# Optimization experiments

Hardware: AMD Instinct MI355X
Metric: run time of the kernel (lower is better)

Reference implementation:

```python
import jax, jax.numpy as jnp
import numpy as np

B, T, D_IN = 64, 256, 256
H, N, W, R, D_OUT = 512, 128, 64, 4, 256
CTRL_IN = D_IN + R * W          # 512
IFACE = R * W + R + W + 1 + W + W + R * 3  # 465
EPS = 1e-8


def setup_inputs() -> dict:
    key = jax.random.key(0)
    ks = jax.random.split(key, 10)
    def lin(k, out_d, in_d):
        s = 1.0 / np.sqrt(in_d)
        return jax.random.uniform(k, (out_d, in_d), jnp.float32, -s, s)
    def vec(k, d, in_d):
        s = 1.0 / np.sqrt(in_d)
        return jax.random.uniform(k, (d,), jnp.float32, -s, s)
    return {
        'x': jax.random.normal(ks[0], (B, T, D_IN), jnp.float32),
        'W_ih': lin(ks[1], 4 * H, CTRL_IN),
        'W_hh': lin(ks[2], 4 * H, H),
        'b_ih': vec(ks[3], 4 * H, H),
        'b_hh': vec(ks[4], 4 * H, H),
        'W_int': lin(ks[5], IFACE, H),
        'b_int': vec(ks[6], IFACE, H),
        'W_out': lin(ks[7], D_OUT, H + R * W),
        'b_out': vec(ks[8], D_OUT, H + R * W),
    }


def _content_weights(mem, keys, strength):
    # mem: (b, n, w); keys: (b, r, w); strength: (b, r, 1) -> weights (b, r, n)
    dot = jnp.einsum('brw,bnw->brn', keys, mem)
    nm = jnp.maximum(jnp.linalg.norm(mem, axis=-1), EPS)      # (b, n)
    nk = jnp.maximum(jnp.linalg.norm(keys, axis=-1), EPS)     # (b, r)
    sim = dot / (nk[:, :, None] * nm[:, None, :])
    return jax.nn.softmax(strength * sim, axis=-1)


def reference(x, W_ih, W_hh, b_ih, b_hh, W_int, b_int, W_out, b_out):
    b = x.shape[0]

    def step(carry, x_t):
        h, c, mem, rv = carry
        ci = jnp.concatenate([x_t, rv.reshape(b, R * W)], axis=-1)
        gates = ci @ W_ih.T + b_ih + h @ W_hh.T + b_hh
        i_g, f_g, g_g, o_g = jnp.split(gates, 4, axis=-1)  # torch LSTM gate order
        c = jax.nn.sigmoid(f_g) * c + jax.nn.sigmoid(i_g) * jnp.tanh(g_g)
        h = jax.nn.sigmoid(o_g) * jnp.tanh(c)

        iface = h @ W_int.T + b_int
        idx = 0
        read_keys = iface[:, idx:idx + R * W].reshape(b, R, W); idx += R * W
        read_str = jax.nn.softplus(iface[:, idx:idx + R]) + 1.0; idx += R
        write_key = iface[:, idx:idx + W]; idx += W
        write_str = jax.nn.softplus(iface[:, idx:idx + 1]) + 1.0; idx += 1
        erase = jax.nn.sigmoid(iface[:, idx:idx + W]); idx += W
        write_vec = iface[:, idx:idx + W]; idx += W
        # read_modes are parsed in the original but never used -> skipped

        ww = _content_weights(mem, write_key[:, None, :], write_str[:, None, :])[:, 0, :]  # (b, n)
        mem = mem * (1.0 - ww[:, :, None] * erase[:, None, :]) + ww[:, :, None] * write_vec[:, None, :]

        rw = _content_weights(mem, read_keys, read_str[:, :, None])  # (b, r, n)
        rv = jnp.einsum('brn,bnw->brw', rw, mem)

        out = jnp.concatenate([h, rv.reshape(b, R * W)], axis=-1) @ W_out.T + b_out
        return (h, c, mem, rv), out

    init = (jnp.zeros((b, H), x.dtype), jnp.zeros((b, H), x.dtype),
            jnp.zeros((b, N, W), x.dtype), jnp.zeros((b, R, W), x.dtype))
    _, outs = jax.lax.scan(step, init, jnp.swapaxes(x, 0, 1))  # outs: (T, b, D_OUT)
    return outs[-1]  # return_sequence=False -> last timestep
```

## Files before the change

### kernel.cpp

```cpp
#include <hip/hip_runtime.h>
#include <math.h>

#define BB_   64
#define TT_   256
#define DIN_  256
#define HH_   512
#define NMEM_ 128
#define WWID_ 64
#define RR_   4
#define DOUT_ 256
#define CTRL_ 512
#define EPSV  1e-8f
#define NBLK  256
#define NTHR  512
#define OSTR  456
#define MPAD  65

__device__ __forceinline__ float sigm(float x){ return 1.f/(1.f+expf(-x)); }
__device__ __forceinline__ float softp(float x){ return (x>20.f)? x : log1pf(expf(x)); }
__device__ __forceinline__ float wredsum(float v){
  #pragma unroll
  for (int o=32;o>0;o>>=1) v += __shfl_xor(v,o,64);
  return v;
}
__device__ __forceinline__ float wredmax(float v){
  #pragma unroll
  for (int o=32;o>0;o>>=1) v = fmaxf(v, __shfl_xor(v,o,64));
  return v;
}

__device__ __forceinline__ float2 cload2(const float* p){
  unsigned long long u = __hip_atomic_load((const unsigned long long*)p,
                          __ATOMIC_RELAXED, __HIP_MEMORY_SCOPE_AGENT);
  float2 r; __builtin_memcpy(&r, &u, 8); return r;
}
__device__ __forceinline__ void cstore2(float* p, float2 v){
  unsigned long long u; __builtin_memcpy(&u, &v, 8);
  __hip_atomic_store((unsigned long long*)p, u, __ATOMIC_RELAXED,
                     __HIP_MEMORY_SCOPE_AGENT);
}
__device__ __forceinline__ void cstore1(float* p, float v){
  unsigned u; __builtin_memcpy(&u, &v, 4);
  __hip_atomic_store((unsigned*)p, u, __ATOMIC_RELAXED, __HIP_MEMORY_SCOPE_AGENT);
}

__device__ __forceinline__ void gridbar(unsigned* bar, unsigned k)
{
  __syncthreads();
  if (threadIdx.x == 0) {
    const int g = blockIdx.x >> 3;
    unsigned a = __hip_atomic_fetch_add(bar + g*32, 1u, __ATOMIC_RELAXED,
                                        __HIP_MEMORY_SCOPE_AGENT);
    bool released = false;
    if (a == 8u*k - 1u) {
      unsigned r = __hip_atomic_fetch_add(bar + 1024, 1u, __ATOMIC_RELAXED,
                                          __HIP_MEMORY_SCOPE_AGENT);
      if (r == 32u*k - 1u) {
        __hip_atomic_store(bar + 1056, k, __ATOMIC_RELAXED,
                           __HIP_MEMORY_SCOPE_AGENT);
        released = true;
      }
    }
    if (!released) {
      while (__hip_atomic_load(bar + 1056, __ATOMIC_RELAXED,
                               __HIP_MEMORY_SCOPE_AGENT) < k)
        __builtin_amdgcn_s_sleep(1);
    }
  }
  __syncthreads();
}

__global__ void k_initbar(unsigned* bar){
  int i = blockIdx.x*256 + threadIdx.x;
  if (i < 1088)
    __hip_atomic_store(bar + i, 0u, __ATOMIC_RELAXED, __HIP_MEMORY_SCOPE_AGENT);
}

__global__ void k_prep_w(const float* __restrict__ Wint, float* __restrict__ WiT4){
  const int o  = blockIdx.x;
  const int kq = threadIdx.x;
  float4 v = *(const float4*)(Wint + (size_t)o*HH_ + 4*kq);
  *(float4*)(WiT4 + ((size_t)kq*OSTR + o)*4) = v;
}

struct Params {
  const float *x, *Wih, *Whh, *bih, *bhh, *bint, *Wout, *bout;
  float *out;
  float *hp;
  float *rvp;
  float *WiT4;
  unsigned *bar;
};

union __align__(16) SMu {
  struct {
    float4 actS[2048];
    float  red[4][4][16][8];
  } a;
  float redO[4][4][64];
  struct {
    float hS[HH_];
    float ifcS[OSTR];
    float kpk[WWID_][8];
    float dH[4][NMEM_];
    float qH[4][NMEM_];
    float nH[4][NMEM_];
    float drH[4][RR_][NMEM_];
    float wwS[NMEM_];
    float rwS[RR_][NMEM_];
    float rvH[8][64];
    float scal[8];
    float red2[8];
  } c;
};

__launch_bounds__(NTHR, 2)
__global__ void k_persist(Params p)
{
  __shared__ SMu sm;
  __shared__ float memS[NMEM_][MPAD];

  const int bi  = blockIdx.x;
  const int tid = threadIdx.x;
  const int b   = tid & 63;
  const int wv  = tid >> 6;
  const int rg  = bi & 31;
  const int col = bi >> 5;
  const int j0  = rg*16;
  const int B0  = col*8;
  const int bb  = bi;

  const int ksA = tid >> 7;
  const int jlA = (tid >> 3) & 15;
  const int blA = tid & 7;

  float c_reg = 0.f;

  const float* wbg[4];
  {
    const float* wsrc = (ksA < 2) ? p.Wih : p.Whh;
    const int koff = (ksA & 1) * 256;
    #pragma unroll
    for (int g = 0; g < 4; ++g)
      wbg[g] = wsrc + (size_t)(g*HH_ + j0 + jlA)*CTRL_ + koff;
  }

  float bsum[4];
  if (tid < 128) {
    const int j = j0 + (tid >> 3);
    #pragma unroll
    for (int g = 0; g < 4; ++g)
      bsum[g] = p.bih[g*HH_ + j] + p.bhh[g*HH_ + j];
  }
  float bintR = 0.f;
  if (bi < 64 && tid < 453) bintR = p.bint[tid];

  {
    const float2 zz = make_float2(0.f, 0.f);
    const int gt = bi*NTHR + tid;
    if      (gt < 16384) cstore2(p.hp  + 2*gt,         zz);
    else if (gt < 24576) cstore2(p.rvp + 2*(gt-16384), zz);
    if (bi < 64)
      for (int i = tid; i < NMEM_*MPAD; i += NTHR)
        ((float*)memS)[i] = 0.f;
  }
  unsigned bk = 1;
  gridbar(p.bar, bk);

  for (int t = 0; t < TT_; ++t) {
    const int cur = t & 1, nxt = cur ^ 1;
    const float* hR = p.hp + cur*32768;
    float*       hW = p.hp + nxt*32768;

    {
      #pragma unroll
      for (int i = 0; i < 4; ++i) {
        const int idx = tid + 512*i;
        const int kq = idx >> 3, bl = idx & 7, bg = B0 + bl;
        float4 v;
        if (kq < 64) {
          v = *(const float4*)(p.x + (size_t)bg*(TT_*DIN_)
                               + (size_t)t*DIN_ + kq*4);
        } else if (kq < 128) {
          const float* s = p.rvp + (kq-64)*256 + bg*4;
          float2 lo = cload2(s), hi = cload2(s + 2);
          v = make_float4(lo.x, lo.y, hi.x, hi.y);
        } else {
          const float* s = hR + (kq-128)*256 + bg*4;
          float2 lo = cload2(s), hi = cload2(s + 2);
          v = make_float4(lo.x, lo.y, hi.x, hi.y);
        }
        sm.a.actS[idx] = v;
      }
      __syncthreads();

      float4 ac[4];
      #pragma unroll
      for (int g = 0; g < 4; ++g) ac[g] = make_float4(0.f, 0.f, 0.f, 0.f);

      const int kbase = ksA*64;
      #pragma unroll 4
      for (int i = 0; i < 64; ++i) {
        float4 a = sm.a.actS[(kbase + i)*8 + blA];
        #pragma unroll
        for (int g = 0; g < 4; ++g) {
          float4 w = *(const float4*)(wbg[g] + (i << 2));
          ac[g].x += w.x*a.x; ac[g].y += w.y*a.y;
          ac[g].z += w.z*a.z; ac[g].w += w.w*a.w;
        }
      }
      #pragma unroll
      for (int g = 0; g < 4; ++g)
        sm.a.red[ksA][g][jlA][blA] = (ac[g].x + ac[g].y) + (ac[g].z + ac[g].w);
      __syncthreads();

      if (tid < 128) {
        const int jl = tid >> 3, bl = tid & 7;
        float gs[4];
        #pragma unroll
        for (int g = 0; g < 4; ++g)
          gs[g] = sm.a.red[0][g][jl][bl] + sm.a.red[1][g][jl][bl]
                + sm.a.red[2][g][jl][bl] + sm.a.red[3][g][jl][bl] + bsum[g];
        float cn = sigm(gs[1])*c_reg + sigm(gs[0])*tanhf(gs[2]);
        c_reg = cn;
        float hn = sigm(gs[3])*tanhf(cn);
        const int j = j0 + jl, bg = B0 + bl;
        cstore1(hW + (j>>2)*256 + bg*4 + (j&3), hn);
      }
    }
    gridbar(p.bar, ++bk);

    if (bi < 64) {
      if (tid < 128) {
        const float* hsrc = hW + tid*256 + bb*4;
        float2 lo = cload2(hsrc), hi = cload2(hsrc + 2);
        sm.c.hS[4*tid]   = lo.x; sm.c.hS[4*tid+1] = lo.y;
        sm.c.hS[4*tid+2] = hi.x; sm.c.hS[4*tid+3] = hi.y;
      }
      __syncthreads();
      {
        const int o = (tid < 453) ? tid : 452;
        float a0 = bintR, a1 = 0.f, a2 = 0.f, a3 = 0.f;
        #pragma unroll 8
        for (int kq = 0; kq < 128; ++kq) {
          float4 w  = *(const float4*)(p.WiT4 + ((size_t)kq*OSTR + o)*4);
          float4 h4 = *(const float4*)&sm.c.hS[kq << 2];
          a0 += w.x*h4.x; a1 += w.y*h4.y; a2 += w.z*h4.z; a3 += w.w*h4.w;
        }
        if (tid < 453) sm.c.ifcS[tid] = (a0 + a1) + (a2 + a3);
      }
      __syncthreads();

      if (tid < 64) {
        const int w = tid;
        float wk = sm.c.ifcS[260+w];
        float q0 = sm.c.ifcS[w],      q1 = sm.c.ifcS[64+w];
        float q2 = sm.c.ifcS[128+w],  q3 = sm.c.ifcS[192+w];
        float er  = sigm(sm.c.ifcS[325+w]);
        float wvc = sm.c.ifcS[389+w];
        sm.c.kpk[w][0]=wk; sm.c.kpk[w][1]=q0; sm.c.kpk[w][2]=q1; sm.c.kpk[w][3]=q2;
        sm.c.kpk[w][4]=q3; sm.c.kpk[w][5]=er; sm.c.kpk[w][6]=wvc; sm.c.kpk[w][7]=0.f;
        float s0 = wredsum(wk*wk);
        float s1 = wredsum(q0*q0);
        float s2 = wredsum(q1*q1);
        float s3 = wredsum(q2*q2);
        float s4 = wredsum(q3*q3);
        if (w == 0) {
          sm.c.scal[0] = fmaxf(sqrtf(s0), EPSV);
          sm.c.scal[1] = fmaxf(sqrtf(s1), EPSV);
          sm.c.scal[2] = fmaxf(sqrtf(s2), EPSV);
          sm.c.scal[3] = fmaxf(sqrtf(s3), EPSV);
          sm.c.scal[4] = fmaxf(sqrtf(s4), EPSV);
        }
      }
      __syncthreads();

      const int n  = tid & 127;
      const int wh = tid >> 7;

      {
        float dotw = 0.f, q = 0.f;
        const int w0 = wh*16;
        #pragma unroll
        for (int w = 0; w < 16; ++w) {
          float m = memS[n][w0+w];
          dotw += sm.c.kpk[w0+w][0]*m;
          q    += m*m;
        }
        sm.c.dH[wh][n] = dotw;
        sm.c.qH[wh][n] = q;
      }
      __syncthreads();

      float a_n = 0.f, e_n = 0.f;
      const float wstr = softp(sm.c.ifcS[324]) + 1.f;
      if (tid < 128) {
        float dot = sm.c.dH[0][n] + sm.c.dH[1][n] + sm.c.dH[2][n] + sm.c.dH[3][n];
        float q2  = sm.c.qH[0][n] + sm.c.qH[1][n] + sm.c.qH[2][n] + sm.c.qH[3][n];
        a_n = wstr * dot / (sm.c.scal[0] * fmaxf(sqrtf(q2), EPSV));
        float mx = wredmax(a_n);
        if ((tid & 63) == 0) sm.c.red2[tid>>6] = mx;
      }
      __syncthreads();
      if (tid < 128) {
        float mx = fmaxf(sm.c.red2[0], sm.c.red2[1]);
        e_n = expf(a_n - mx);
        float s = wredsum(e_n);
        if ((tid & 63) == 0) sm.c.red2[4 + (tid>>6)] = s;
      }
      __syncthreads();
      if (tid < 128)
        sm.c.wwS[n] = e_n / (sm.c.red2[4] + sm.c.red2[5]);
      __syncthreads();

      {
        float ww_n = sm.c.wwS[n];
        float nrm=0.f, d0=0.f, d1=0.f, d2=0.f, d3=0.f;
        const int w0 = wh*16;
        #pragma unroll
        for (int w = 0; w < 16; ++w) {
          float4 k0 = *(const float4*)&sm.c.kpk[w0+w][0];
          float4 k1 = *(const float4*)&sm.c.kpk[w0+w][4];
          float m  = memS[n][w0+w];
          float mn = m*(1.f - ww_n*k1.y) + ww_n*k1.z;
          memS[n][w0+w] = mn;
          nrm += mn*mn;
          d0 += k0.y*mn; d1 += k0.z*mn; d2 += k0.w*mn; d3 += k1.x*mn;
        }
        sm.c.nH[wh][n] = nrm;
        sm.c.drH[wh][0][n]=d0; sm.c.drH[wh][1][n]=d1;
        sm.c.drH[wh][2][n]=d2; sm.c.drH[wh][3][n]=d3;
      }
      __syncthreads();

      if (tid < 128) {
        float nrm = sm.c.nH[0][n] + sm.c.nH[1][n] + sm.c.nH[2][n] + sm.c.nH[3][n];
        float inm = 1.f / fmaxf(sqrtf(nrm), EPSV);
        #pragma unroll
        for (int r = 0; r < RR_; ++r) {
          float rstr = softp(sm.c.ifcS[256+r]) + 1.f;
          float dr = sm.c.drH[0][r][n] + sm.c.drH[1][r][n]
                   + sm.c.drH[2][r][n] + sm.c.drH[3][r][n];
          sm.c.rwS[r][n] = rstr * dr * inm / sm.c.scal[1+r];
        }
      }
      __syncthreads();

      if (tid < 256) {
        float v0 = sm.c.rwS[wv][b], v1 = sm.c.rwS[wv][b+64];
        float mx = wredmax(fmaxf(v0, v1));
        float e0 = expf(v0-mx), e1 = expf(v1-mx);
        float s  = wredsum(e0+e1);
        sm.c.rwS[wv][b]    = e0/s;
        sm.c.rwS[wv][b+64] = e1/s;
      }
      __syncthreads();

      {
        const int r  = wv >> 1;
        const int n0 = (wv & 1) * 64;
        float acc = 0.f;
        #pragma unroll 4
        for (int n2 = n0; n2 < n0 + 64; n2 += 4) {
          float4 r4 = *(const float4*)&sm.c.rwS[r][n2];
          acc += r4.x*memS[n2][b]   + r4.y*memS[n2+1][b]
               + r4.z*memS[n2+2][b] + r4.w*memS[n2+3][b];
        }
        sm.c.rvH[wv][b] = acc;
      }
      __syncthreads();
      if (tid < 256) {
        const int r = tid >> 6;
        float acc = sm.c.rvH[2*r][b] + sm.c.rvH[2*r+1][b];
        const int k = r*64 + b;
        cstore1(p.rvp + (k>>2)*256 + bb*4 + (k&3), acc);
      }
    }
    gridbar(p.bar, ++bk);
  }

  if (bi < 64) {
    const int o0 = bi*4;
    if (tid < 256) {
      float acc[4] = {0.f, 0.f, 0.f, 0.f};
      #pragma unroll 4
      for (int kk = 0; kk < 48; ++kk) {
        const int k = wv*192 + kk*4;
        const float* a8 = (k < 512)
          ? (p.hp  + (((k    )>>2)*64 + b)*4)
          : (p.rvp + (((k-512)>>2)*64 + b)*4);
        float2 alo = cload2(a8);
        float2 ahi = cload2(a8 + 2);
        #pragma unroll
        for (int r = 0; r < 4; ++r) {
          float4 w = *(const float4*)(p.Wout + (size_t)(o0+r)*(HH_ + RR_*WWID_) + k);
          acc[r] += w.x*alo.x + w.y*alo.y + w.z*ahi.x + w.w*ahi.y;
        }
      }
      #pragma unroll
      for (int r = 0; r < 4; ++r) sm.redO[wv][r][b] = acc[r];
    }
    __syncthreads();
    if (tid < 64) {
      float4 o4;
      float* po = (float*)&o4;
      #pragma unroll
      for (int r = 0; r < 4; ++r)
        po[r] = sm.redO[0][r][b] + sm.redO[1][r][b] + sm.redO[2][r][b]
              + sm.redO[3][r][b] + p.bout[o0+r];
      *(float4*)(p.out + (size_t)b*DOUT_ + o0) = o4;
    }
  }
}

extern "C" void kernel_launch(void* const* d_in, const int* in_sizes, int n_in,
                              void* d_out, int out_size, void* d_ws, size_t ws_size,
                              hipStream_t stream)
{
  Params prm;
  prm.x    = (const float*)d_in[0];
  prm.Wih  = (const float*)d_in[1];
  prm.Whh  = (const float*)d_in[2];
  prm.bih  = (const float*)d_in[3];
  prm.bhh  = (const float*)d_in[4];
  const float* Wint = (const float*)d_in[5];
  prm.bint = (const float*)d_in[6];
  prm.Wout = (const float*)d_in[7];
  prm.bout = (const float*)d_in[8];
  prm.out  = (float*)d_out;

  float* ws = (float*)d_ws;
  size_t off = 0;
  prm.hp   = ws + off; off += 2*32768;
  prm.rvp  = ws + off; off += 16384;
  prm.WiT4 = ws + off; off += (size_t)128*OSTR*4;
  prm.bar  = (unsigned*)(ws + off); off += 2048;

  k_prep_w<<<453, 128, 0, stream>>>(Wint, prm.WiT4);
  k_initbar<<<5, 256, 0, stream>>>(prm.bar);
  k_persist<<<NBLK, NTHR, 0, stream>>>(prm);
}
```

Measured before the change: 8.562 ms.

## Replace global grid barriers with per-column producer/consumer counters

Swaps the two full-grid barriers per timestep for column-local counters. Each group of 32 blocks working on 8 batch rows signals the LSTM phase through colA, and the 8 memory-phase blocks of that column signal completion through colC. The memory-phase work is remapped so each column's batch rows are handled by blocks in that same column. This is meant to cut the cost of global synchronisation and let columns drift out of lockstep. In exchange it makes the ordering logic more delicate, relying on relaxed atomics and a final wait across all columns before the output projection.

After: 8.318 ms. -2.8%, faster.

```diff
diff --git a/kernel.cpp b/kernel.cpp
--- a/kernel.cpp
+++ b/kernel.cpp
@@ -43,36 +43,16 @@
   unsigned u; __builtin_memcpy(&u, &v, 4);
   __hip_atomic_store((unsigned*)p, u, __ATOMIC_RELAXED, __HIP_MEMORY_SCOPE_AGENT);
 }
-
-__device__ __forceinline__ void gridbar(unsigned* bar, unsigned k)
-{
-  __syncthreads();
-  if (threadIdx.x == 0) {
-    const int g = blockIdx.x >> 3;
-    unsigned a = __hip_atomic_fetch_add(bar + g*32, 1u, __ATOMIC_RELAXED,
-                                        __HIP_MEMORY_SCOPE_AGENT);
-    bool released = false;
-    if (a == 8u*k - 1u) {
-      unsigned r = __hip_atomic_fetch_add(bar + 1024, 1u, __ATOMIC_RELAXED,
-                                          __HIP_MEMORY_SCOPE_AGENT);
-      if (r == 32u*k - 1u) {
-        __hip_atomic_store(bar + 1056, k, __ATOMIC_RELAXED,
-                           __HIP_MEMORY_SCOPE_AGENT);
-        released = true;
-      }
-    }
-    if (!released) {
-      while (__hip_atomic_load(bar + 1056, __ATOMIC_RELAXED,
-                               __HIP_MEMORY_SCOPE_AGENT) < k)
-        __builtin_amdgcn_s_sleep(1);
-    }
-  }
-  __syncthreads();
+__device__ __forceinline__ unsigned cloadu(const unsigned* p){
+  return __hip_atomic_load(p, __ATOMIC_RELAXED, __HIP_MEMORY_SCOPE_AGENT);
+}
+__device__ __forceinline__ void cincr(unsigned* p){
+  __hip_atomic_fetch_add(p, 1u, __ATOMIC_RELAXED, __HIP_MEMORY_SCOPE_AGENT);
 }
 
 __global__ void k_initbar(unsigned* bar){
   int i = blockIdx.x*256 + threadIdx.x;
-  if (i < 1088)
+  if (i < 576)
     __hip_atomic_store(bar + i, 0u, __ATOMIC_RELAXED, __HIP_MEMORY_SCOPE_AGENT);
 }
 
@@ -128,7 +108,11 @@
   const int col = bi >> 5;
   const int j0  = rg*16;
   const int B0  = col*8;
-  const int bb  = bi;
+  const bool isBC = (rg < 8);
+  const int bb  = col*8 + rg;
+
+  unsigned* colA = p.bar + col*32;
+  unsigned* colC = p.bar + 256 + col*32;
 
   const int ksA = tid >> 7;
   const int jlA = (tid >> 3) & 15;
@@ -153,24 +137,34 @@
       bsum[g] = p.bih[g*HH_ + j] + p.bhh[g*HH_ + j];
   }
   float bintR = 0.f;
-  if (bi < 64 && tid < 453) bintR = p.bint[tid];
+  if (isBC && tid < 453) bintR = p.bint[tid];
 
   {
     const float2 zz = make_float2(0.f, 0.f);
     const int gt = bi*NTHR + tid;
     if      (gt < 16384) cstore2(p.hp  + 2*gt,         zz);
     else if (gt < 24576) cstore2(p.rvp + 2*(gt-16384), zz);
-    if (bi < 64)
+    if (isBC)
       for (int i = tid; i < NMEM_*MPAD; i += NTHR)
         ((float*)memS)[i] = 0.f;
   }
-  unsigned bk = 1;
-  gridbar(p.bar, bk);
+  __syncthreads();
+  if (tid == 0) {
+    cincr(p.bar + 512);
+    while (cloadu(p.bar + 512) < (unsigned)NBLK) __builtin_amdgcn_s_sleep(2);
+  }
+  __syncthreads();
 
   for (int t = 0; t < TT_; ++t) {
     const int cur = t & 1, nxt = cur ^ 1;
     const float* hR = p.hp + cur*32768;
     float*       hW = p.hp + nxt*32768;
+
+    if (t > 0) {
+      if (tid == 0)
+        while (cloadu(colC) < 8u*(unsigned)t) __builtin_amdgcn_s_sleep(1);
+      __syncthreads();
+    }
 
     {
       #pragma unroll
@@ -228,9 +222,14 @@
         cstore1(hW + (j>>2)*256 + bg*4 + (j&3), hn);
       }
     }
-    gridbar(p.bar, ++bk);
-
-    if (bi < 64) {
+    __syncthreads();
+    if (tid == 0) cincr(colA);
+
+    if (isBC) {
+      if (tid == 0)
+        while (cloadu(colA) < 32u*(unsigned)(t+1)) __builtin_amdgcn_s_sleep(1);
+      __syncthreads();
+
       if (tid < 128) {
         const float* hsrc = hW + tid*256 + bb*4;
         float2 lo = cload2(hsrc), hi = cload2(hsrc + 2);
@@ -375,11 +374,19 @@
         const int k = r*64 + b;
         cstore1(p.rvp + (k>>2)*256 + bb*4 + (k&3), acc);
       }
-    }
-    gridbar(p.bar, ++bk);
+      __syncthreads();
+      if (tid == 0) cincr(colC);
+    }
   }
 
   if (bi < 64) {
+    if (tid == 0) {
+      #pragma unroll
+      for (int c2 = 0; c2 < 8; ++c2)
+        while (cloadu(p.bar + 256 + c2*32) < 8u*(unsigned)TT_)
+          __builtin_amdgcn_s_sleep(1);
+    }
+    __syncthreads();
     const int o0 = bi*4;
     if (tid < 256) {
       float acc[4] = {0.f, 0.f, 0.f, 0.f};
@@ -434,9 +441,9 @@
   prm.hp   = ws + off; off += 2*32768;
   prm.rvp  = ws + off; off += 16384;
   prm.WiT4 = ws + off; off += (size_t)128*OSTR*4;
-  prm.bar  = (unsigned*)(ws + off); off += 2048;
+  prm.bar  = (unsigned*)(ws + off); off += 1024;
 
   k_prep_w<<<453, 128, 0, stream>>>(Wint, prm.WiT4);
-  k_initbar<<<5, 256, 0, stream>>>(prm.bar);
+  k_initbar<<<3, 256, 0, stream>>>(prm.bar);
   k_persist<<<NBLK, NTHR, 0, stream>>>(prm);
 }
```
